# Optimization experiments

Hardware: AMD Instinct MI355X
Metric: run time of the kernel (lower is better)

The kernel has to match this reference:

```python
import jax, jax.numpy as jnp
import numpy as np

K = 3      # kernel_size
PAD = 1    # padding
HID = 64   # hidden
EPS = 1e-5

def _unfold(x, H, W):
    # x: (B, CT, H, W) -> (B, CT, K*K, H*W); matches torch nn.Unfold channel-major layout
    xp = jnp.pad(x, ((0, 0), (0, 0), (PAD, PAD), (PAD, PAD)))
    patches = jnp.stack([xp[:, :, i:i + H, j:j + W]
                         for i in range(K) for j in range(K)], axis=2)
    B, CT = x.shape[:2]
    return patches.reshape(B, CT, K * K, H * W)

def _fold(y, H, W):
    # y: (B, CT, K*K, H*W) -> scatter-add overlapping patches -> (B, CT, H, W); matches F.fold
    B, CT = y.shape[:2]
    y = y.reshape(B, CT, K * K, H, W)
    out = jnp.zeros((B, CT, H + 2 * PAD, W + 2 * PAD), y.dtype)
    idx = 0
    for i in range(K):
        for j in range(K):
            out = out.at[:, :, i:i + H, j:j + W].add(y[:, :, idx])
            idx += 1
    return out[:, :, PAD:PAD + H, PAD:PAD + W]

def setup_inputs() -> dict:
    key = jax.random.key(0)
    ks = jax.random.split(key, 4)
    B, C, T, H, W = 8, 64, 4, 56, 56
    return {
        "x": jax.random.normal(ks[0], (B, C, T, H, W), jnp.float32),
        "w_in": jax.random.normal(ks[1], (3 * HID, C), jnp.float32) * (C ** -0.5),
        "b_in": jnp.zeros((3 * HID,), jnp.float32),
        "w_out": jax.random.normal(ks[2], (C, HID), jnp.float32) * (HID ** -0.5),
        "b_out": jnp.zeros((C,), jnp.float32),
        "gamma": jnp.ones((C,), jnp.float32),
        "beta": jnp.zeros((C,), jnp.float32),
    }

def reference(x, w_in, b_in, w_out, b_out, gamma, beta):
    B, C, T, H, W = x.shape
    k2 = K * K
    # 1x1x1 conv_in -> theta, phi, g
    h = jnp.einsum('oc,bcthw->bothw', w_in, x) + b_in[None, :, None, None, None]
    theta, phi, g = jnp.split(h, 3, axis=1)

    def unf(z):  # (B, HID, T, H, W) -> (B, HID, T*k2, H*W)
        z = z.reshape(B, HID * T, H, W)
        return _unfold(z, H, W).reshape(B, HID, T * k2, H * W)

    tu, pu, gu = unf(theta), unf(phi), unf(g)
    # per-spatial-location attention over T*k2 axis; dot_product normalization
    attn = jnp.einsum('bcts,bcps->btps', tu, pu) / (T * k2)
    out = jnp.einsum('btgs,bcgs->bcts', attn, gu)      # (B, HID, T*k2, H*W)
    out = out.reshape(B, HID * T, k2, H * W)
    out = _fold(out, H, W).reshape(B, HID, T, H, W)
    # 1x1x1 conv_out
    out = jnp.einsum('oc,bcthw->bothw', w_out, out) + b_out[None, :, None, None, None]
    # BatchNorm3d (training-mode batch statistics, biased variance)
    mu = out.mean(axis=(0, 2, 3, 4), keepdims=True)
    var = out.var(axis=(0, 2, 3, 4), keepdims=True)
    out = (out - mu) * jax.lax.rsqrt(var + EPS)
    out = out * gamma[None, :, None, None, None] + beta[None, :, None, None, None]
    return x + out
```

## Files before the change

kernel.cpp:

```cpp
#include <hip/hip_runtime.h>


typedef unsigned short u16;
typedef unsigned int u32;
using f32x4 = __attribute__((ext_vector_type(4))) float;
using bf16x8 = __attribute__((ext_vector_type(8))) short;

#define BB 8
#define TT 4
#define HH 56
#define HWD 3136
#define GROW 64
#define GPLANE 3584
#define NTOT 100352.0f

__device__ __forceinline__ float bf_lo(u32 u) { return __uint_as_float(u << 16); }
__device__ __forceinline__ float bf_hi(u32 u) { return __uint_as_float(u & 0xffff0000u); }
__device__ __forceinline__ float bf16u(u16 u) { return __uint_as_float(((u32)u) << 16); }
__device__ __forceinline__ u16 f2bf(float f) {
  u32 u = __float_as_uint(f);
  u32 r = (u + 0x7fffu + ((u >> 16) & 1u)) >> 16;
  return (u16)r;
}
__device__ __forceinline__ u32 pack2(float a, float b) {
  return (u32)f2bf(a) | ((u32)f2bf(b) << 16);
}
__device__ __forceinline__ int imax(int a, int b) { return a > b ? a : b; }
__device__ __forceinline__ int imin(int a, int b) { return a < b ? a : b; }
__device__ __forceinline__ float cntf(int d, int p) {
  int lo = imax(-1, imax(-1 - d, p - (HH - 1)));
  int hi = imin(1, imin(1 - d, p));
  int n = hi - lo + 1;
  return n > 0 ? (float)n : 0.f;
}

#define K1_XOFF 24576
__global__ __launch_bounds__(256, 4) void k_conv_in(const float* __restrict__ x,
                                                    const float* __restrict__ w_in,
                                                    const float* __restrict__ b_in,
                                                    u16* __restrict__ th, u16* __restrict__ ph,
                                                    u16* __restrict__ g2, float* __restrict__ stats) {
  __shared__ __align__(16) char sm[24576 + 8192];
  if (blockIdx.x == 0 && threadIdx.x < 128) stats[threadIdx.x] = 0.f;
  int bt = blockIdx.x / 49, chunk = blockIdx.x % 49;
  int b = bt >> 2, t = bt & 3;
  int p0 = chunk * 64;
  int tid = threadIdx.x;

#pragma unroll
  for (int it = 0; it < 12; ++it) {
    int task = it * 256 + tid;
    int o = task >> 4, c4 = (task & 15) * 4;
    float4 wv = *reinterpret_cast<const float4*>(&w_in[o * 64 + c4]);
    uint2 pv;
    pv.x = pack2(wv.x, wv.y);
    pv.y = pack2(wv.z, wv.w);
    *reinterpret_cast<uint2*>(sm + o * 128 + ((c4 * 2) ^ ((o & 7) << 4))) = pv;
  }
  const float* xb = x + ((size_t)b * 256 + t) * HWD + p0;
#pragma unroll
  for (int it = 0; it < 2; ++it) {
    int task = it * 256 + tid;
    int cp = task >> 4, p4 = task & 15;
    int c0 = cp * 2;
    float4 fa = *reinterpret_cast<const float4*>(&xb[(size_t)c0 * 4 * HWD + p4 * 4]);
    float4 fb = *reinterpret_cast<const float4*>(&xb[(size_t)(c0 + 1) * 4 * HWD + p4 * 4]);
    float va[4] = {fa.x, fa.y, fa.z, fa.w}, vb[4] = {fb.x, fb.y, fb.z, fb.w};
#pragma unroll
    for (int j = 0; j < 4; ++j) {
      int p = p4 * 4 + j;
      int slot = (p & 7) ^ ((p >> 2) & 7);
      *reinterpret_cast<u32*>(sm + K1_XOFF + p * 128 + ((c0 * 2) ^ (slot << 4))) = pack2(va[j], vb[j]);
    }
  }
  __syncthreads();

  int w = tid >> 6, lane = tid & 63, lr = lane & 15, lk = lane >> 4;
  f32x4 acc[3][4];
#pragma unroll
  for (int i = 0; i < 3; ++i)
#pragma unroll
    for (int n = 0; n < 4; ++n) acc[i][n] = (f32x4){0.f, 0.f, 0.f, 0.f};

#pragma unroll
  for (int kt = 0; kt < 2; ++kt) {
    bf16x8 af[3], bfr[4];
#pragma unroll
    for (int i = 0; i < 3; ++i) {
      int arow = (w * 3 + i) * 16 + lr;
      af[i] = *reinterpret_cast<const bf16x8*>(sm + arow * 128 + ((kt * 64 + lk * 16) ^ ((arow & 7) << 4)));
    }
#pragma unroll
    for (int n = 0; n < 4; ++n) {
      int brow = n * 16 + lr;
      int slot = (brow & 7) ^ ((brow >> 2) & 7);
      bfr[n] = *reinterpret_cast<const bf16x8*>(sm + K1_XOFF + brow * 128 + ((kt * 64 + lk * 16) ^ (slot << 4)));
    }
#pragma unroll
    for (int i = 0; i < 3; ++i)
#pragma unroll
      for (int n = 0; n < 4; ++n)
        acc[i][n] = __builtin_amdgcn_mfma_f32_16x16x32_bf16(af[i], bfr[n], acc[i][n], 0, 0, 0);
  }

#pragma unroll
  for (int i = 0; i < 3; ++i) {
    int mt = w * 3 + i;
    int ob = mt * 16 + lk * 4;
    int gsel = ob >> 6, o = ob & 63;
    float4 bv = *reinterpret_cast<const float4*>(&b_in[ob]);
    if (gsel < 2) {
      u16* og = gsel == 0 ? th : ph;
#pragma unroll
      for (int n = 0; n < 4; ++n) {
        int p = p0 + n * 16 + lr;
        f32x4 a = acc[i][n];
        uint2 v;
        v.x = pack2(a.x + bv.x, a.y + bv.y);
        v.y = pack2(a.z + bv.z, a.w + bv.w);
        *reinterpret_cast<uint2*>(&og[((size_t)bt * HWD + p) * 64 + o]) = v;
      }
    } else {
      float bb[4] = {bv.x, bv.y, bv.z, bv.w};
      int y0p = p0 / 56;
      int rel0 = p0 - y0p * 56;
#pragma unroll
      for (int n = 0; n < 4; ++n) {
        f32x4 a = acc[i][n];
        float aa[4] = {a.x, a.y, a.z, a.w};
        int rel = rel0 + n * 16 + lr;
        int cnd = rel >= 56;
        int off = (y0p + cnd) * GROW + (rel - (cnd ? 56 : 0)) + 2;
#pragma unroll
        for (int r = 0; r < 4; ++r)
          g2[(((size_t)b * 64 + o + r) * 4 + t) * GPLANE + off] = f2bf(aa[r] + bb[r]);
      }
    }
  }
}

#define PH_OFF 0
#define AS_OFF 0
#define G_OFF 32768
#define W_OFF 32768
#define TH_OFF 65536
#define FOLD_OFF 65536
#define TAB_OFF 73728

__global__ __launch_bounds__(512, 4) void k_attn(const u16* __restrict__ th, const u16* __restrict__ ph,
                                                 const u16* __restrict__ g2,
                                                 const float* __restrict__ w_out,
                                                 const float* __restrict__ b_out,
                                                 u16* __restrict__ pre) {
  __shared__ __align__(16) char sm[73984];

  int bi0 = blockIdx.x;
  int bi = (bi0 & 7) * 196 + (bi0 >> 3);
  int b = bi / 196, tile = bi % 196;
  int ty = tile / 14, tx = tile % 14;
  int y0 = ty * 4, x0 = tx * 4;
  int tid = threadIdx.x;
  int w = tid >> 6, lane = tid & 63;
  int lr = lane & 15, lk = lane >> 4;

  for (int task = tid; task < 2048; task += 512) {
    int row = task >> 3, ch = task & 7;
    int rho = row >> 6, Z = row & 63, zy = Z >> 3, zx = Z & 7;
    int Y = y0 - 2 + zy, X = x0 - 2 + zx;
    uint4 v = make_uint4(0, 0, 0, 0);
    if ((unsigned)Y < HH && (unsigned)X < HH)
      v = *reinterpret_cast<const uint4*>(&ph[(((size_t)b * 4 + rho) * HWD + Y * HH + X) * 64 + ch * 8]);
    *reinterpret_cast<uint4*>(sm + PH_OFF + row * 128 + ((ch * 16) ^ ((row & 7) << 4))) = v;
  }
  {
    int row = tid >> 3, ch = tid & 7;
    int pos = row >> 2, tau = row & 3;
    int Y = y0 + (pos >> 2), X = x0 + (pos & 3);
    uint4 v = *reinterpret_cast<const uint4*>(&th[(((size_t)b * 4 + tau) * HWD + Y * HH + X) * 64 + ch * 8]);
    *reinterpret_cast<uint4*>(sm + TH_OFF + row * 128 + ((ch * 16) ^ ((row & 7) << 4))) = v;
  }
  for (int task = tid; task < 2048; task += 512) {
    int c = task >> 5, rho = (task >> 3) & 3, zy = task & 7;
    int Y = y0 - 2 + zy;
    uint2 lo = make_uint2(0, 0), hi = make_uint2(0, 0);
    if ((unsigned)Y < HH) {
      const u16* gb = g2 + (((size_t)b * 64 + c) * 4 + rho) * GPLANE + Y * GROW + x0;
      lo = *reinterpret_cast<const uint2*>(gb);
      hi = *reinterpret_cast<const uint2*>(gb + 4);
    }
    uint4 v = make_uint4(lo.x, lo.y, hi.x, hi.y);
    *reinterpret_cast<uint4*>(sm + G_OFF + c * 512 + ((16 * (rho * 8 + zy)) ^ ((c & 7) << 4))) = v;
  }
  if (tid < 32) {
    int zy = tid >> 2, py = tid & 3;
    reinterpret_cast<float*>(sm + TAB_OFF)[tid] = cntf(zy - 2 - py, y0 + py) * (1.f / 36.f);
  } else if (tid < 64) {
    int i = tid - 32;
    int zx = i >> 2, px = i & 3;
    reinterpret_cast<float*>(sm + TAB_OFF + 128)[i] = cntf(zx - 2 - px, x0 + px);
  }
  __syncthreads();

  bf16x8 tb[4][2];
#pragma unroll
  for (int nt = 0; nt < 4; ++nt)
#pragma unroll
    for (int kt = 0; kt < 2; ++kt) {
      int row = nt * 16 + lr;
      tb[nt][kt] = *reinterpret_cast<const bf16x8*>(sm + TH_OFF + row * 128 + ((kt * 64 + lk * 16) ^ ((row & 7) << 4)));
    }
  f32x4 accA[2][4];
#pragma unroll
  for (int mi = 0; mi < 2; ++mi)
#pragma unroll
    for (int nt = 0; nt < 4; ++nt) accA[mi][nt] = (f32x4){0.f, 0.f, 0.f, 0.f};
  __builtin_amdgcn_s_setprio(1);
#pragma unroll
  for (int mi = 0; mi < 2; ++mi) {
    int mt = w * 2 + mi;
    int mrow = mt * 16 + lr;
    int p2 = (2 * mt) & 7;
#pragma unroll
    for (int kt = 0; kt < 2; ++kt) {
      bf16x8 af = *reinterpret_cast<const bf16x8*>(sm + PH_OFF + mrow * 128 + ((kt * 64 + lk * 16) ^ ((mrow & 7) << 4)));
#pragma unroll
      for (int nt = 0; nt < 4; ++nt) {
        if ((p2 == 0 && nt >= 2) || (p2 == 6 && nt < 2)) continue;
        accA[mi][nt] = __builtin_amdgcn_mfma_f32_16x16x32_bf16(af, tb[nt][kt], accA[mi][nt], 0, 0, 0);
      }
    }
  }
  __builtin_amdgcn_s_setprio(0);
  __syncthreads();

  {
    const float* cyt = reinterpret_cast<const float*>(sm + TAB_OFF);
    const float* cxt = reinterpret_cast<const float*>(sm + TAB_OFF + 128);
    int px = lr >> 2;
#pragma unroll
    for (int mi = 0; mi < 2; ++mi) {
      int mbase = (w * 2 + mi) * 16 + lk * 4;
      int zy = (mbase >> 3) & 7;
      int zxb = mbase & 7;
      float cxv[4];
#pragma unroll
      for (int r = 0; r < 4; ++r) cxv[r] = cxt[(zxb + r) * 4 + px];
#pragma unroll
      for (int nt = 0; nt < 4; ++nt) {
        int n = nt * 16 + lr;
        float cyv = cyt[zy * 4 + nt];
        f32x4 a = accA[mi][nt];
        uint2 vv;
        vv.x = pack2(a.x * cyv * cxv[0], a.y * cyv * cxv[1]);
        vv.y = pack2(a.z * cyv * cxv[2], a.w * cyv * cxv[3]);
        *reinterpret_cast<uint2*>(sm + AS_OFF + n * 512 + ((mbase * 2) ^ ((n & 7) << 4))) = vv;
      }
    }
  }
  __syncthreads();

  int mtB = w & 3, ntb = (w >> 2) * 2;
  f32x4 accB[2];
  accB[0] = (f32x4){0.f, 0.f, 0.f, 0.f};
  accB[1] = (f32x4){0.f, 0.f, 0.f, 0.f};
  {
    int arow = mtB * 16 + lr;
    __builtin_amdgcn_s_setprio(1);
#pragma unroll
    for (int kt = 0; kt < 8; ++kt) {
      bf16x8 af = *reinterpret_cast<const bf16x8*>(sm + AS_OFF + arow * 512 + ((kt * 64 + lk * 16) ^ ((arow & 7) << 4)));
#pragma unroll
      for (int j = 0; j < 2; ++j) {
        int brow = (ntb + j) * 16 + lr;
        bf16x8 bfv = *reinterpret_cast<const bf16x8*>(sm + G_OFF + brow * 512 + ((kt * 64 + lk * 16) ^ ((brow & 7) << 4)));
        accB[j] = __builtin_amdgcn_mfma_f32_16x16x32_bf16(af, bfv, accB[j], 0, 0, 0);
      }
    }
    __builtin_amdgcn_s_setprio(0);
  }
  __syncthreads();

#pragma unroll
  for (int j = 0; j < 2; ++j) {
    int n = (ntb + j) * 16 + lr;
#pragma unroll
    for (int r = 0; r < 4; ++r) {
      int m = mtB * 16 + lk * 4 + r;
      *reinterpret_cast<u16*>(sm + FOLD_OFF + m * 128 + ((n * 2) ^ ((m & 7) << 4))) = f2bf(accB[j][r]);
    }
  }
  {
    int o = tid >> 3, cg = tid & 7;
    float4 w0 = *reinterpret_cast<const float4*>(&w_out[o * 64 + cg * 8]);
    float4 w1 = *reinterpret_cast<const float4*>(&w_out[o * 64 + cg * 8 + 4]);
    uint4 wv = make_uint4(pack2(w0.x, w0.y), pack2(w0.z, w0.w), pack2(w1.x, w1.y), pack2(w1.z, w1.w));
    *reinterpret_cast<uint4*>(sm + W_OFF + o * 128 + ((cg * 16) ^ ((o & 7) << 4))) = wv;
  }
  __syncthreads();

  int mtC = w & 3, ntc = (w >> 2) * 2;
  f32x4 accC[2];
  accC[0] = (f32x4){0.f, 0.f, 0.f, 0.f};
  accC[1] = (f32x4){0.f, 0.f, 0.f, 0.f};
  {
    int arow = mtC * 16 + lr;
    __builtin_amdgcn_s_setprio(1);
#pragma unroll
    for (int kt = 0; kt < 2; ++kt) {
      bf16x8 af = *reinterpret_cast<const bf16x8*>(sm + W_OFF + arow * 128 + ((kt * 64 + lk * 16) ^ ((arow & 7) << 4)));
#pragma unroll
      for (int j = 0; j < 2; ++j) {
        int brow = (ntc + j) * 16 + lr;
        bf16x8 bfv = *reinterpret_cast<const bf16x8*>(sm + FOLD_OFF + brow * 128 + ((kt * 64 + lk * 16) ^ ((brow & 7) << 4)));
        accC[j] = __builtin_amdgcn_mfma_f32_16x16x32_bf16(af, bfv, accC[j], 0, 0, 0);
      }
    }
    __builtin_amdgcn_s_setprio(0);
  }
  {
    int o = mtC * 16 + lk * 4;
    float4 bo = *reinterpret_cast<const float4*>(&b_out[o]);
#pragma unroll
    for (int j = 0; j < 2; ++j) {
      int n = (ntc + j) * 16 + lr;
      int pos = n >> 2, tau = n & 3;
      int hw = (y0 + (pos >> 2)) * HH + x0 + (pos & 3);
      uint2 v;
      v.x = pack2(accC[j].x + bo.x, accC[j].y + bo.y);
      v.y = pack2(accC[j].z + bo.z, accC[j].w + bo.w);
      *reinterpret_cast<uint2*>(&pre[(((size_t)b * 4 + tau) * HWD + hw) * 64 + o]) = v;
    }
  }
}

__global__ __launch_bounds__(256) void k_stats(const u16* __restrict__ pre, float* __restrict__ stats) {
  __shared__ float rs[8][64], qs[8][64];
  int tid = threadIdx.x;
  int og = tid & 31, pg = tid >> 5;
  const u32* p32 = reinterpret_cast<const u32*>(pre);
  size_t base = (size_t)blockIdx.x * 256 + pg * 32;
  float s0 = 0.f, s1 = 0.f, q0 = 0.f, q1 = 0.f;
#pragma unroll 4
  for (int j = 0; j < 32; ++j) {
    u32 v = p32[(base + j) * 32 + og];
    float a = bf_lo(v), c = bf_hi(v);
    s0 += a; q0 += a * a;
    s1 += c; q1 += c * c;
  }
  rs[pg][og * 2] = s0; rs[pg][og * 2 + 1] = s1;
  qs[pg][og * 2] = q0; qs[pg][og * 2 + 1] = q1;
  __syncthreads();
  if (tid < 64) {
    float ts = 0.f, tq = 0.f;
#pragma unroll
    for (int g = 0; g < 8; ++g) { ts += rs[g][tid]; tq += qs[g][tid]; }
    atomicAdd(&stats[tid], ts);
    atomicAdd(&stats[64 + tid], tq);
  }
}

__global__ __launch_bounds__(256) void k_final(const float* __restrict__ x, const u16* __restrict__ pre,
                                               const float* __restrict__ stats,
                                               const float* __restrict__ gamma,
                                               const float* __restrict__ beta,
                                               float* __restrict__ out) {
  __shared__ u32 pt[32][65];
  int bi = blockIdx.x;
  int bt = bi / 49, ck = bi % 49;
  int b = bt >> 2, t = bt & 3;
  int hw0 = ck * 64;
  int tid = threadIdx.x;
  const u32* src = reinterpret_cast<const u32*>(pre) + ((size_t)bt * HWD + hw0) * 32;
#pragma unroll
  for (int it = 0; it < 8; ++it) {
    int task = it * 256 + tid;
    int p = task >> 5, cu = task & 31;
    pt[cu][p] = src[p * 32 + cu];
  }
  __syncthreads();
  int slot = tid & 15, c2 = tid >> 4;
  int p4 = slot * 4;
  const float invN = 1.f / NTOT;
#pragma unroll
  for (int half = 0; half < 2; ++half) {
    int cp = c2 + half * 16;
    int c0 = cp * 2;
    float mu0 = stats[c0] * invN;
    float va0 = stats[64 + c0] * invN - mu0 * mu0;
    float s0 = rsqrtf(va0 + 1e-5f) * gamma[c0];
    float h0 = beta[c0] - mu0 * s0;
    float mu1 = stats[c0 + 1] * invN;
    float va1 = stats[64 + c0 + 1] * invN - mu1 * mu1;
    float s1 = rsqrtf(va1 + 1e-5f) * gamma[c0 + 1];
    float h1 = beta[c0 + 1] - mu1 * s1;
    uint4 pv = *reinterpret_cast<const uint4*>(&pt[cp][p4]);
    size_t xb0 = ((size_t)(b * 64 + c0) * 4 + t) * HWD + hw0 + p4;
    size_t xb1 = xb0 + 4 * HWD;
    float4 x0v = *reinterpret_cast<const float4*>(&x[xb0]);
    float4 x1v = *reinterpret_cast<const float4*>(&x[xb1]);
    float4 o0, o1;
    o0.x = x0v.x + bf_lo(pv.x) * s0 + h0;  o1.x = x1v.x + bf_hi(pv.x) * s1 + h1;
    o0.y = x0v.y + bf_lo(pv.y) * s0 + h0;  o1.y = x1v.y + bf_hi(pv.y) * s1 + h1;
    o0.z = x0v.z + bf_lo(pv.z) * s0 + h0;  o1.z = x1v.z + bf_hi(pv.z) * s1 + h1;
    o0.w = x0v.w + bf_lo(pv.w) * s0 + h0;  o1.w = x1v.w + bf_hi(pv.w) * s1 + h1;
    *reinterpret_cast<float4*>(&out[xb0]) = o0;
    *reinterpret_cast<float4*>(&out[xb1]) = o1;
  }
}

extern "C" void kernel_launch(void* const* d_in, const int* in_sizes, int n_in,
                              void* d_out, int out_size, void* d_ws, size_t ws_size,
                              hipStream_t stream) {
  const float* x = (const float*)d_in[0];
  const float* w_in = (const float*)d_in[1];
  const float* b_in = (const float*)d_in[2];
  const float* w_out = (const float*)d_in[3];
  const float* b_out = (const float*)d_in[4];
  const float* gamma = (const float*)d_in[5];
  const float* beta = (const float*)d_in[6];
  float* out = (float*)d_out;

  const size_t NE = (size_t)BB * TT * HWD * 64;
  const size_t NG = (size_t)BB * 64 * TT * GPLANE;
  u16* th = (u16*)d_ws;
  u16* ph = th + NE;
  u16* g2 = ph + NE;
  u16* pre = g2 + NG;
  float* stats = (float*)(pre + NE);

  k_conv_in<<<dim3(BB * TT * 49), dim3(256), 0, stream>>>(x, w_in, b_in, th, ph, g2, stats);
  k_attn<<<dim3(BB * 196), dim3(512), 0, stream>>>(th, ph, g2, w_out, b_out, pre);
  k_stats<<<dim3(392), dim3(256), 0, stream>>>(pre, stats);
  k_final<<<dim3(BB * TT * 49), dim3(256), 0, stream>>>(x, pre, stats, gamma, beta, out);
}
```

Before: 79.97 us.

## Store pre-norm output channel-major and simplify stats and final kernels

The attention kernel now writes its conv_out result in (B, C, T, HW) layout with scalar 16-bit stores instead of the channel-last packed layout. This lets the stats kernel reduce one channel per block with wave shuffles, and lets the final kernel do a straight elementwise pass without an LDS transpose. Block indices in conv_in and final are also remapped with an XCD-style interleave. The cost is scattered 2-byte stores in the attention epilogue, which may hurt write coalescing.

Measured after the change: 74.29 us. 1.08x faster.

```diff
diff --git a/kernel.cpp b/kernel.cpp
--- a/kernel.cpp
+++ b/kernel.cpp
@@ -42,7 +42,9 @@
                                                     u16* __restrict__ g2, float* __restrict__ stats) {
   __shared__ __align__(16) char sm[24576 + 8192];
   if (blockIdx.x == 0 && threadIdx.x < 128) stats[threadIdx.x] = 0.f;
-  int bt = blockIdx.x / 49, chunk = blockIdx.x % 49;
+  int bi0 = blockIdx.x;
+  int bi = (bi0 & 7) * 196 + (bi0 >> 3);
+  int bt = bi / 49, chunk = bi % 49;
   int b = bt >> 2, t = bt & 3;
   int p0 = chunk * 64;
   int tid = threadIdx.x;
@@ -318,44 +320,54 @@
     __builtin_amdgcn_s_setprio(0);
   }
   {
-    int o = mtC * 16 + lk * 4;
-    float4 bo = *reinterpret_cast<const float4*>(&b_out[o]);
+    int o4 = mtC * 16 + lk * 4;
+    float4 bo = *reinterpret_cast<const float4*>(&b_out[o4]);
+    float bof[4] = {bo.x, bo.y, bo.z, bo.w};
 #pragma unroll
     for (int j = 0; j < 2; ++j) {
       int n = (ntc + j) * 16 + lr;
       int pos = n >> 2, tau = n & 3;
       int hw = (y0 + (pos >> 2)) * HH + x0 + (pos & 3);
-      uint2 v;
-      v.x = pack2(accC[j].x + bo.x, accC[j].y + bo.y);
-      v.y = pack2(accC[j].z + bo.z, accC[j].w + bo.w);
-      *reinterpret_cast<uint2*>(&pre[(((size_t)b * 4 + tau) * HWD + hw) * 64 + o]) = v;
+      float av[4] = {accC[j].x, accC[j].y, accC[j].z, accC[j].w};
+#pragma unroll
+      for (int r = 0; r < 4; ++r)
+        pre[((size_t)(b * 64 + o4 + r) * 4 + tau) * HWD + hw] = f2bf(av[r] + bof[r]);
     }
   }
 }
 
 __global__ __launch_bounds__(256) void k_stats(const u16* __restrict__ pre, float* __restrict__ stats) {
-  __shared__ float rs[8][64], qs[8][64];
+  __shared__ float rs[4], rq[4];
   int tid = threadIdx.x;
-  int og = tid & 31, pg = tid >> 5;
-  const u32* p32 = reinterpret_cast<const u32*>(pre);
-  size_t base = (size_t)blockIdx.x * 256 + pg * 32;
-  float s0 = 0.f, s1 = 0.f, q0 = 0.f, q1 = 0.f;
-#pragma unroll 4
-  for (int j = 0; j < 32; ++j) {
-    u32 v = p32[(base + j) * 32 + og];
-    float a = bf_lo(v), c = bf_hi(v);
-    s0 += a; q0 += a * a;
-    s1 += c; q1 += c * c;
-  }
-  rs[pg][og * 2] = s0; rs[pg][og * 2 + 1] = s1;
-  qs[pg][og * 2] = q0; qs[pg][og * 2 + 1] = q1;
-  __syncthreads();
-  if (tid < 64) {
-    float ts = 0.f, tq = 0.f;
-#pragma unroll
-    for (int g = 0; g < 8; ++g) { ts += rs[g][tid]; tq += qs[g][tid]; }
-    atomicAdd(&stats[tid], ts);
-    atomicAdd(&stats[64 + tid], tq);
+  int b = blockIdx.x & 7, c = blockIdx.x >> 3;
+  const uint4* p = reinterpret_cast<const uint4*>(pre + (size_t)(b * 64 + c) * 4 * HWD);
+  float s = 0.f, q = 0.f;
+#pragma unroll
+  for (int j = 0; j < 7; ++j) {
+    int idx = j * 256 + tid;
+    if (idx < 1568) {
+      uint4 v = p[idx];
+      u32 uu[4] = {v.x, v.y, v.z, v.w};
+#pragma unroll
+      for (int k = 0; k < 4; ++k) {
+        float a = bf_lo(uu[k]), d = bf_hi(uu[k]);
+        s += a + d;
+        q += a * a + d * d;
+      }
+    }
+  }
+#pragma unroll
+  for (int off = 32; off; off >>= 1) {
+    s += __shfl_down(s, off);
+    q += __shfl_down(q, off);
+  }
+  if ((tid & 63) == 0) { rs[tid >> 6] = s; rq[tid >> 6] = q; }
+  __syncthreads();
+  if (tid == 0) {
+    float ts = rs[0] + rs[1] + rs[2] + rs[3];
+    float tq = rq[0] + rq[1] + rq[2] + rq[3];
+    atomicAdd(&stats[c], ts);
+    atomicAdd(&stats[64 + c], tq);
   }
 }
 
@@ -364,48 +376,25 @@
                                                const float* __restrict__ gamma,
                                                const float* __restrict__ beta,
                                                float* __restrict__ out) {
-  __shared__ u32 pt[32][65];
-  int bi = blockIdx.x;
-  int bt = bi / 49, ck = bi % 49;
-  int b = bt >> 2, t = bt & 3;
-  int hw0 = ck * 64;
-  int tid = threadIdx.x;
-  const u32* src = reinterpret_cast<const u32*>(pre) + ((size_t)bt * HWD + hw0) * 32;
-#pragma unroll
-  for (int it = 0; it < 8; ++it) {
-    int task = it * 256 + tid;
-    int p = task >> 5, cu = task & 31;
-    pt[cu][p] = src[p * 32 + cu];
-  }
-  __syncthreads();
-  int slot = tid & 15, c2 = tid >> 4;
-  int p4 = slot * 4;
+  int bi0 = blockIdx.x;
+  int bi = (bi0 & 7) * 392 + (bi0 >> 3);
+  size_t i8 = ((size_t)bi * 256 + threadIdx.x) * 8;
+  int c = (int)((i8 / 12544) & 63);
   const float invN = 1.f / NTOT;
-#pragma unroll
-  for (int half = 0; half < 2; ++half) {
-    int cp = c2 + half * 16;
-    int c0 = cp * 2;
-    float mu0 = stats[c0] * invN;
-    float va0 = stats[64 + c0] * invN - mu0 * mu0;
-    float s0 = rsqrtf(va0 + 1e-5f) * gamma[c0];
-    float h0 = beta[c0] - mu0 * s0;
-    float mu1 = stats[c0 + 1] * invN;
-    float va1 = stats[64 + c0 + 1] * invN - mu1 * mu1;
-    float s1 = rsqrtf(va1 + 1e-5f) * gamma[c0 + 1];
-    float h1 = beta[c0 + 1] - mu1 * s1;
-    uint4 pv = *reinterpret_cast<const uint4*>(&pt[cp][p4]);
-    size_t xb0 = ((size_t)(b * 64 + c0) * 4 + t) * HWD + hw0 + p4;
-    size_t xb1 = xb0 + 4 * HWD;
-    float4 x0v = *reinterpret_cast<const float4*>(&x[xb0]);
-    float4 x1v = *reinterpret_cast<const float4*>(&x[xb1]);
-    float4 o0, o1;
-    o0.x = x0v.x + bf_lo(pv.x) * s0 + h0;  o1.x = x1v.x + bf_hi(pv.x) * s1 + h1;
-    o0.y = x0v.y + bf_lo(pv.y) * s0 + h0;  o1.y = x1v.y + bf_hi(pv.y) * s1 + h1;
-    o0.z = x0v.z + bf_lo(pv.z) * s0 + h0;  o1.z = x1v.z + bf_hi(pv.z) * s1 + h1;
-    o0.w = x0v.w + bf_lo(pv.w) * s0 + h0;  o1.w = x1v.w + bf_hi(pv.w) * s1 + h1;
-    *reinterpret_cast<float4*>(&out[xb0]) = o0;
-    *reinterpret_cast<float4*>(&out[xb1]) = o1;
-  }
+  float mu = stats[c] * invN;
+  float var = stats[64 + c] * invN - mu * mu;
+  float s = rsqrtf(var + 1e-5f) * gamma[c];
+  float h = beta[c] - mu * s;
+  uint4 pv = *reinterpret_cast<const uint4*>(&pre[i8]);
+  float4 xa = *reinterpret_cast<const float4*>(&x[i8]);
+  float4 xbv = *reinterpret_cast<const float4*>(&x[i8 + 4]);
+  float4 o0, o1;
+  o0.x = xa.x + bf_lo(pv.x) * s + h;   o0.y = xa.y + bf_hi(pv.x) * s + h;
+  o0.z = xa.z + bf_lo(pv.y) * s + h;   o0.w = xa.w + bf_hi(pv.y) * s + h;
+  o1.x = xbv.x + bf_lo(pv.z) * s + h;  o1.y = xbv.y + bf_hi(pv.z) * s + h;
+  o1.z = xbv.z + bf_lo(pv.w) * s + h;  o1.w = xbv.w + bf_hi(pv.w) * s + h;
+  *reinterpret_cast<float4*>(&out[i8]) = o0;
+  *reinterpret_cast<float4*>(&out[i8 + 4]) = o1;
 }
 
 extern "C" void kernel_launch(void* const* d_in, const int* in_sizes, int n_in,
@@ -430,6 +419,6 @@
 
   k_conv_in<<<dim3(BB * TT * 49), dim3(256), 0, stream>>>(x, w_in, b_in, th, ph, g2, stats);
   k_attn<<<dim3(BB * 196), dim3(512), 0, stream>>>(th, ph, g2, w_out, b_out, pre);
-  k_stats<<<dim3(392), dim3(256), 0, stream>>>(pre, stats);
-  k_final<<<dim3(BB * TT * 49), dim3(256), 0, stream>>>(x, pre, stats, gamma, beta, out);
-}
+  k_stats<<<dim3(512), dim3(256), 0, stream>>>(pre, stats);
+  k_final<<<dim3(3136), dim3(256), 0, stream>>>(x, pre, stats, gamma, beta, out);
+}
```
